# Performance work log

Measured on AMD Instinct MI355X. Metric: run time of the kernel, lower is better.

## Reference

```python
import jax, jax.numpy as jnp
import numpy as np

B, S, D = 4, 2048, 1024
DFF = 4096        # dense FFN hidden
E, DFE = 8, 1024  # n_experts, expert hidden
K = 2             # top-k routing
LAM = 0.5         # coe_lambda


def setup_inputs() -> dict:
    key = jax.random.key(0)
    ks = jax.random.split(key, 10)
    s = 0.02
    return {
        "x":   jax.random.normal(ks[0], (B, S, D), jnp.float32),
        "W1":  jax.random.normal(ks[1], (D, DFF), jnp.float32) * s,
        "b1":  jnp.zeros((DFF,), jnp.float32),
        "W2":  jax.random.normal(ks[2], (DFF, D), jnp.float32) * s,
        "b2":  jnp.zeros((D,), jnp.float32),
        "Wg":  jax.random.normal(ks[3], (D, E), jnp.float32) * s,
        "We1": jax.random.normal(ks[4], (E, D, DFE), jnp.float32) * s,
        "be1": jnp.zeros((E, DFE), jnp.float32),
        "We2": jax.random.normal(ks[5], (E, DFE, D), jnp.float32) * s,
        "be2": jnp.zeros((E, D), jnp.float32),
        "id":  S // 2,  # python int cutoff: tokens < id are FFN-only
    }


def reference(x, W1, b1, W2, b2, Wg, We1, be1, We2, be2, id):
    # Dense FFN applied to every token (both branches compute it).
    ffn_out = jax.nn.gelu(x @ W1 + b1) @ W2 + b2                   # [B,S,D]

    # MoE: softmax router, top-k renormalized gates.
    probs = jax.nn.softmax(x @ Wg, axis=-1)                        # [B,S,E]
    topv, topi = jax.lax.top_k(probs, K)                           # [B,S,K]
    topv = topv / topv.sum(-1, keepdims=True)
    gates = (jax.nn.one_hot(topi, E, dtype=x.dtype) * topv[..., None]).sum(-2)  # [B,S,E]

    # All-expert dense evaluation, then gated combine.
    h = jax.nn.gelu(jnp.einsum('bsd,edf->bsef', x, We1) + be1)     # [B,S,E,DFE]
    eo = jnp.einsum('bsef,efd->bsed', h, We2) + be2                # [B,S,E,D]
    moe_out = jnp.einsum('bse,bsed->bsd', gates, eo)               # [B,S,D]

    # Branch selection: token i < id (and S != 1) -> FFN only; else FFN + lam*MoE.
    seq = x.shape[1]
    mask = ((jnp.arange(seq) >= id) | (seq == 1)).astype(x.dtype)  # [S]
    return ffn_out + LAM * mask[None, :, None] * moe_out
```

## Files before the change

kernel.cpp:

```cpp
#include <hip/hip_runtime.h>
#include <hip/hip_bf16.h>
#include <cstdint>
#include <cstddef>

typedef unsigned short ushort_t;
typedef __bf16 bf16x8v __attribute__((ext_vector_type(8)));
typedef float f32x4 __attribute__((ext_vector_type(4)));

#define Bsz 4
#define Sseq 2048
#define Dd 1024
#define DFFd 4096
#define Ee 8
#define DFEd 1024
#define IDCUT 1024
#define NTOK (Bsz*Sseq)
#define NMOE (Bsz*(Sseq-IDCUT))
#define MAXSLOT 4096

__device__ __forceinline__ ushort_t f2bf(float f) {
  unsigned u = __float_as_uint(f);
  u += 0x7fffu + ((u >> 16) & 1u);
  return (ushort_t)(u >> 16);
}

__device__ __forceinline__ unsigned pk2bf(float a, float b) {
  return (unsigned)f2bf(a) | ((unsigned)f2bf(b) << 16);
}

__device__ __forceinline__ float gelu_f(float x) {
  float u = x * (1.0f + 0.044715f * x * x);
  float s = 1.0f / (1.0f + __expf(-1.5957691216057308f * u));
  return x * s;
}

__device__ __forceinline__ void gload_lds16(const void* g, void* l) {
  __builtin_amdgcn_global_load_lds(
      (const __attribute__((address_space(1))) void*)g,
      (__attribute__((address_space(3))) void*)l,
      16, 0, 0);
}

__device__ __forceinline__ void cast_dev(const float* __restrict__ x,
                                         ushort_t* __restrict__ xb, int wg) {
  const int row  = wg * 4 + (threadIdx.x >> 6);
  const int lane = threadIdx.x & 63;
  const float* xr = x + (size_t)row * Dd;
  ushort_t* xbr = xb + (size_t)row * Dd;
  float4 v[4];
  #pragma unroll
  for (int j = 0; j < 4; ++j) v[j] = ((const float4*)xr)[lane + j * 64];
  #pragma unroll
  for (int j = 0; j < 4; ++j) {
    ushort4 o;
    o.x = f2bf(v[j].x); o.y = f2bf(v[j].y); o.z = f2bf(v[j].z); o.w = f2bf(v[j].w);
    ((ushort4*)xbr)[lane + j * 64] = o;
  }
}

__device__ __forceinline__ void router_dev(
    const float* __restrict__ x, const float* __restrict__ Wg,
    int* __restrict__ cnt, int* __restrict__ slots, float* __restrict__ gsv,
    int blk, int* __restrict__ eTok, int* __restrict__ lbase)
{
  const int wid = threadIdx.x >> 6, lane = threadIdx.x & 63;
  const int tblk = blk * 64;

  #pragma unroll 1
  for (int it = 0; it < 16; ++it) {
    const int ti = it * 4 + wid;
    const int t  = tblk + ti;
    const int b  = t >> 10, s = (t & 1023) + IDCUT;
    const float* xr = x + ((size_t)b * Sseq + s) * Dd;
    float4 accA = {0.f,0.f,0.f,0.f}, accB = {0.f,0.f,0.f,0.f};
    #pragma unroll
    for (int j = 0; j < 4; ++j) {
      const float4 v = ((const float4*)xr)[lane + j * 64];
      const int kbase = (lane + j * 64) * 4;
      #pragma unroll
      for (int r = 0; r < 4; ++r) {
        const float xv = (r == 0) ? v.x : (r == 1) ? v.y : (r == 2) ? v.z : v.w;
        const float4 wa = *(const float4*)(Wg + (size_t)(kbase + r) * 8);
        const float4 wb = *(const float4*)(Wg + (size_t)(kbase + r) * 8 + 4);
        accA.x += xv * wa.x; accA.y += xv * wa.y; accA.z += xv * wa.z; accA.w += xv * wa.w;
        accB.x += xv * wb.x; accB.y += xv * wb.y; accB.z += xv * wb.z; accB.w += xv * wb.w;
      }
    }
    float acc[8] = {accA.x, accA.y, accA.z, accA.w, accB.x, accB.y, accB.z, accB.w};
    #pragma unroll
    for (int off = 32; off > 0; off >>= 1) {
      #pragma unroll
      for (int e8 = 0; e8 < 8; ++e8) acc[e8] += __shfl_xor(acc[e8], off);
    }
    if (lane == 0) {
      int e0 = 0; float v0 = acc[0];
      #pragma unroll
      for (int e8 = 1; e8 < 8; ++e8) if (acc[e8] > v0) { v0 = acc[e8]; e0 = e8; }
      int e1 = -1; float v1 = -3.4e38f;
      #pragma unroll
      for (int e8 = 0; e8 < 8; ++e8) if (e8 != e0 && acc[e8] > v1) { v1 = acc[e8]; e1 = e8; }
      float g0 = 1.0f / (1.0f + expf(v1 - v0));
      eTok[ti * 2] = e0; eTok[ti * 2 + 1] = e1;
      gsv[t * 2] = g0;  gsv[t * 2 + 1] = 1.0f - g0;
    }
  }
  __syncthreads();
  if (wid == 0) {
    int cnts[8] = {0,0,0,0,0,0,0,0};
    int el[2];
    #pragma unroll
    for (int p = 0; p < 2; ++p) {
      el[p] = eTok[p * 64 + lane];
      #pragma unroll
      for (int e = 0; e < 8; ++e)
        cnts[e] += __popcll(__ballot(el[p] == e));
    }
    if (lane < 8) lbase[lane] = atomicAdd(&cnt[lane], cnts[lane]);
    int run[8];
    #pragma unroll
    for (int e = 0; e < 8; ++e) run[e] = lbase[e];
    #pragma unroll
    for (int p = 0; p < 2; ++p) {
      const int ent = p * 64 + lane;
      const int val = (tblk + (ent >> 1)) * 2 + (ent & 1);
      #pragma unroll
      for (int e = 0; e < 8; ++e) {
        unsigned long long m = __ballot(el[p] == e);
        if (el[p] == e)
          slots[e * MAXSLOT + run[e] + __popcll(m & ((1ull << lane) - 1ull))] = val;
        run[e] += __popcll(m);
      }
    }
  }
}

__device__ __forceinline__ void t64x128(const float* __restrict__ in,
                                        ushort_t* __restrict__ out,
                                        int R, int C, int by, int bx,
                                        float* __restrict__ lds) {
  const int t = threadIdx.x;
  const int c4 = t & 31;
  const int r0 = t >> 5;
  const float* src = in + (size_t)(by * 64) * C + bx * 128;
  #pragma unroll
  for (int p = 0; p < 8; ++p) {
    const int r = r0 + p * 8;
    const float4 vv = *(const float4*)(src + (size_t)r * C + c4 * 4);
    *(float4*)(lds + r * 129 + c4 * 4) = vv;
  }
  __syncthreads();
  ushort_t* dst = out + (size_t)(bx * 128) * R + by * 64;
  const int rr0 = (t & 7) * 8;
  #pragma unroll
  for (int p = 0; p < 4; ++p) {
    const int cc = (t >> 3) + p * 32;
    const float* col = lds + (size_t)rr0 * 129 + cc;
    float f0 = col[0*129], f1 = col[1*129], f2 = col[2*129], f3 = col[3*129];
    float f4 = col[4*129], f5 = col[5*129], f6 = col[6*129], f7 = col[7*129];
    uint4 q;
    q.x = pk2bf(f0, f1); q.y = pk2bf(f2, f3);
    q.z = pk2bf(f4, f5); q.w = pk2bf(f6, f7);
    *(uint4*)(dst + (size_t)cc * R + rr0) = q;
  }
}

__global__ __launch_bounds__(256) void prep1_k(
    const float* __restrict__ x, ushort_t* __restrict__ xb,
    const float* __restrict__ Wg,
    int* __restrict__ cnt, int* __restrict__ slots, float* __restrict__ gsv,
    const float* __restrict__ W1, ushort_t* __restrict__ W1t,
    const float* __restrict__ We1, ushort_t* __restrict__ We1t)
{
  __shared__ char smemraw[64 * 129 * 4];
  const int wg = blockIdx.x;
  if (wg < 2048) {
    cast_dev(x, xb, wg);
  } else if (wg < 2112) {
    router_dev(x, Wg, cnt, slots, gsv, wg - 2048,
               (int*)smemraw, (int*)(smemraw + 512));
  } else if (wg < 2624) {
    const int i = wg - 2112;
    t64x128(W1, W1t, Dd, DFFd, i >> 5, i & 31, (float*)smemraw);
  } else {
    const int i = wg - 2624, z = i >> 7, rem = i & 127;
    t64x128(We1 + (size_t)z * Dd * DFEd, We1t + (size_t)z * Dd * DFEd,
            Dd, DFEd, rem >> 3, rem & 7, (float*)smemraw);
  }
}

template<int MODE>
__device__ __forceinline__ void gemm_tile(
    int nt, int mt, int e,
    const ushort_t* __restrict__ A, const ushort_t* __restrict__ Bt,
    const float* __restrict__ biase, void* __restrict__ C,
    int M, int lda, int N, int ldc,
    const int* __restrict__ cnt, const int* __restrict__ slots,
    const float* __restrict__ gates,
    ushort_t* Al, ushort_t* Bl)
{
  int rows = M;
  const int* slist = nullptr;
  if (MODE >= 2) {
    rows = cnt[e];
    if (mt * 128 >= rows) return;
    slist = slots + e * MAXSLOT;
  }
  const ushort_t* Bte = (MODE >= 2) ? (Bt + (size_t)e * (size_t)lda * (size_t)N) : Bt;

  const int tid  = threadIdx.x;
  const int lane = tid & 63;
  const int wid  = tid >> 6;
  const int wr   = wid >> 1, wc = wid & 1;
  const int lr   = lane & 15;
  const int lg   = lane >> 4;
  const int swz7 = lane & 7;

  const ushort_t* gA[4];
  const ushort_t* gB[4];
  #pragma unroll
  for (int j = 0; j < 4; ++j) {
    int tt = j * 256 + tid;
    int rl = tt >> 3, slot = tt & 7;
    int col8 = slot ^ (rl & 7);
    int grow = mt * 128 + rl;
    size_t rowoff;
    if (MODE < 2) {
      rowoff = (size_t)grow;
    } else {
      int idx = grow > rows - 1 ? rows - 1 : grow;
      int sv = slist[idx];
      if (MODE == 2) { int t = sv >> 1; rowoff = (size_t)((t >> 10) * Sseq + IDCUT + (t & 1023)); }
      else           { rowoff = (size_t)sv; }
    }
    gA[j] = A + rowoff * (size_t)lda + col8 * 8;
    gB[j] = Bte + (size_t)(nt * 128 + rl) * (size_t)lda + col8 * 8;
  }

  f32x4 acc[4][4];
  const f32x4 vzero = {0.f, 0.f, 0.f, 0.f};
  #pragma unroll
  for (int m = 0; m < 4; ++m)
    #pragma unroll
    for (int n = 0; n < 4; ++n) acc[m][n] = vzero;

  const unsigned aRow = (unsigned)((wr * 64 + lr) * 128);
  const unsigned bRow = (unsigned)((wc * 64 + lr) * 128);
  const unsigned s0 = (unsigned)((lg ^ swz7) << 4);
  const unsigned s1 = (unsigned)(((4 + lg) ^ swz7) << 4);

  for (int k0 = 0; k0 < lda; k0 += 64) {
    __syncthreads();
    #pragma unroll
    for (int j = 0; j < 4; ++j)
      gload_lds16(gA[j] + k0, (void*)((char*)Al + (j * 256 + wid * 64) * 16));
    #pragma unroll
    for (int j = 0; j < 4; ++j)
      gload_lds16(gB[j] + k0, (void*)((char*)Bl + (j * 256 + wid * 64) * 16));
    __syncthreads();

    {
      bf16x8v af[4], bfr[4];
      #pragma unroll
      for (int mi = 0; mi < 4; ++mi)
        af[mi] = *(const bf16x8v*)((const char*)Al + aRow + mi * 2048 + s0);
      #pragma unroll
      for (int ni = 0; ni < 4; ++ni)
        bfr[ni] = *(const bf16x8v*)((const char*)Bl + bRow + ni * 2048 + s0);
      #pragma unroll
      for (int mi = 0; mi < 4; ++mi)
        #pragma unroll
        for (int ni = 0; ni < 4; ++ni)
          acc[mi][ni] = __builtin_amdgcn_mfma_f32_16x16x32_bf16(
              af[mi], bfr[ni], acc[mi][ni], 0, 0, 0);
    }
    {
      bf16x8v af[4], bfr[4];
      #pragma unroll
      for (int mi = 0; mi < 4; ++mi)
        af[mi] = *(const bf16x8v*)((const char*)Al + aRow + mi * 2048 + s1);
      #pragma unroll
      for (int ni = 0; ni < 4; ++ni)
        bfr[ni] = *(const bf16x8v*)((const char*)Bl + bRow + ni * 2048 + s1);
      #pragma unroll
      for (int mi = 0; mi < 4; ++mi)
        #pragma unroll
        for (int ni = 0; ni < 4; ++ni)
          acc[mi][ni] = __builtin_amdgcn_mfma_f32_16x16x32_bf16(
              af[mi], bfr[ni], acc[mi][ni], 0, 0, 0);
    }
  }

  #pragma unroll
  for (int mf = 0; mf < 4; ++mf) {
    #pragma unroll
    for (int jj = 0; jj < 4; ++jj) {
      const int lrow = wr * 64 + mf * 16 + lg * 4 + jj;
      const int grow = mt * 128 + lrow;
      size_t crow; float gt = 0.f;
      if (MODE >= 2) {
        if (grow >= rows) continue;
        int sv = slist[grow];
        if (MODE == 3) {
          gt = gates[sv];
          int tkn = sv >> 1;
          crow = (size_t)((tkn >> 10) * Sseq + IDCUT + (tkn & 1023));
        } else {
          crow = (size_t)sv;
        }
      } else {
        crow = (size_t)grow;
      }
      #pragma unroll
      for (int nf = 0; nf < 4; ++nf) {
        const int gcol = nt * 128 + wc * 64 + nf * 16 + lr;
        float v = acc[mf][nf][jj] + biase[gcol];
        if (MODE == 0 || MODE == 2) {
          ((ushort_t*)C)[crow * (size_t)ldc + gcol] = f2bf(gelu_f(v));
        } else if (MODE == 1) {
          ((float*)C)[crow * (size_t)ldc + gcol] = v;
        } else {
          atomicAdd(&((float*)C)[crow * (size_t)ldc + gcol], 0.5f * gt * v);
        }
      }
    }
  }
}

__global__ __launch_bounds__(256, 3) void fused1_k(
    const ushort_t* __restrict__ xb,
    const ushort_t* __restrict__ W1t, const float* __restrict__ b1, ushort_t* __restrict__ h1,
    const ushort_t* __restrict__ We1t, const float* __restrict__ be1, ushort_t* __restrict__ hs,
    const int* __restrict__ cnt, const int* __restrict__ slots,
    const float* __restrict__ W2, ushort_t* __restrict__ W2t,
    const float* __restrict__ We2, ushort_t* __restrict__ We2t)
{
  __shared__ char smemraw[64 * 129 * 4];
  ushort_t* Al = (ushort_t*)smemraw;
  ushort_t* Bl = (ushort_t*)(smemraw + 16384);
  int wg = blockIdx.x;
  if (wg < 2048) {
    int xcd = wg & 7, idx = wg >> 3;
    int ntB = idx >> 6, mtL = (idx >> 3) & 7, ntS = idx & 7;
    int mt = xcd * 8 + mtL, nt = ntB * 8 + ntS;
    gemm_tile<0>(nt, mt, 0, xb, W1t, b1, (void*)h1, NTOK, Dd, DFFd, DFFd,
                 nullptr, nullptr, nullptr, Al, Bl);
  } else if (wg < 4096) {
    int i = wg - 2048;
    int e = i & 7, j = i >> 3;
    int mt = j >> 3, nt = j & 7;
    gemm_tile<2>(nt, mt, e, xb, We1t, be1 + e * DFEd, (void*)hs, 0, Dd, DFEd, DFEd,
                 cnt, slots, nullptr, Al, Bl);
  } else if (wg < 4608) {
    const int i = wg - 4096;
    t64x128(W2, W2t, DFFd, Dd, i >> 3, i & 7, (float*)smemraw);
  } else {
    const int i = wg - 4608, z = i >> 7, rem = i & 127;
    t64x128(We2 + (size_t)z * DFEd * Dd, We2t + (size_t)z * DFEd * Dd,
            DFEd, Dd, rem >> 3, rem & 7, (float*)smemraw);
  }
}

__global__ __launch_bounds__(256, 3) void ffn2_k(
    const ushort_t* __restrict__ h1,
    const ushort_t* __restrict__ W2t, const float* __restrict__ b2,
    float* __restrict__ out)
{
  __shared__ ushort_t Al[128 * 64];
  __shared__ ushort_t Bl[128 * 64];
  int wg = blockIdx.x;
  int xcd = wg & 7, idx = wg >> 3;
  int nt = idx >> 3, mtL = idx & 7;
  int mt = xcd * 8 + mtL;
  gemm_tile<1>(nt, mt, 0, h1, W2t, b2, (void*)out, NTOK, DFFd, Dd, Dd,
               nullptr, nullptr, nullptr, Al, Bl);
}

__global__ __launch_bounds__(256, 3) void moe2_k(
    const ushort_t* __restrict__ hs,
    const ushort_t* __restrict__ We2t, const float* __restrict__ be2,
    float* __restrict__ out,
    const int* __restrict__ cnt, const int* __restrict__ slots,
    const float* __restrict__ gsv)
{
  __shared__ ushort_t Al[128 * 64];
  __shared__ ushort_t Bl[128 * 64];
  int wg = blockIdx.x;
  int e = wg & 7, j = wg >> 3;
  int mt = j >> 3, nt = j & 7;
  gemm_tile<3>(nt, mt, e, hs, We2t, be2 + e * Dd, (void*)out, 0, DFEd, Dd, Dd,
               cnt, slots, gsv, Al, Bl);
}

#define WS_XB    ((size_t)0)
#define WS_W1T   ((size_t)16777216)
#define WS_W2T   ((size_t)25165824)
#define WS_WE1T  ((size_t)33554432)
#define WS_WE2T  ((size_t)50331648)
#define WS_H1    ((size_t)67108864)
#define WS_HS    ((size_t)134217728)
#define WS_CNT   ((size_t)184549376)
#define WS_SLOT  ((size_t)184549632)
#define WS_GSV   ((size_t)184680704)

extern "C" void kernel_launch(void* const* d_in, const int* in_sizes, int n_in,
                              void* d_out, int out_size, void* d_ws, size_t ws_size,
                              hipStream_t stream) {
  const float* x   = (const float*)d_in[0];
  const float* W1  = (const float*)d_in[1];
  const float* b1  = (const float*)d_in[2];
  const float* W2  = (const float*)d_in[3];
  const float* b2  = (const float*)d_in[4];
  const float* Wg  = (const float*)d_in[5];
  const float* We1 = (const float*)d_in[6];
  const float* be1 = (const float*)d_in[7];
  const float* We2 = (const float*)d_in[8];
  const float* be2 = (const float*)d_in[9];
  float* out = (float*)d_out;

  char* ws = (char*)d_ws;
  ushort_t* xb   = (ushort_t*)(ws + WS_XB);
  ushort_t* W1t  = (ushort_t*)(ws + WS_W1T);
  ushort_t* W2t  = (ushort_t*)(ws + WS_W2T);
  ushort_t* We1t = (ushort_t*)(ws + WS_WE1T);
  ushort_t* We2t = (ushort_t*)(ws + WS_WE2T);
  ushort_t* h1   = (ushort_t*)(ws + WS_H1);
  ushort_t* hs   = (ushort_t*)(ws + WS_HS);
  int*      cnt  = (int*)(ws + WS_CNT);
  int*      slots= (int*)(ws + WS_SLOT);
  float*    gsv  = (float*)(ws + WS_GSV);

  hipMemsetAsync(cnt, 0, 8 * sizeof(int), stream);

  prep1_k<<<dim3(3648), 256, 0, stream>>>(x, xb, Wg, cnt, slots, gsv,
                                          W1, W1t, We1, We1t);
  fused1_k<<<dim3(5632), 256, 0, stream>>>(xb, W1t, b1, h1, We1t, be1, hs,
                                           cnt, slots, W2, W2t, We2, We2t);
  ffn2_k<<<dim3(512), 256, 0, stream>>>(h1, W2t, b2, out);
  moe2_k<<<dim3(2048), 256, 0, stream>>>(hs, We2t, be2, out, cnt, slots, gsv);
}
```

Before: 292.9 us.

## Merge FFN2 and MoE2 GEMMs into one launch; replace atomics with staged combine

```diff
diff --git a/kernel.cpp b/kernel.cpp
--- a/kernel.cpp
+++ b/kernel.cpp
@@ -300,13 +300,8 @@
       if (MODE >= 2) {
         if (grow >= rows) continue;
         int sv = slist[grow];
-        if (MODE == 3) {
-          gt = gates[sv];
-          int tkn = sv >> 1;
-          crow = (size_t)((tkn >> 10) * Sseq + IDCUT + (tkn & 1023));
-        } else {
-          crow = (size_t)sv;
-        }
+        crow = (size_t)sv;
+        if (MODE == 3) gt = gates[sv];
       } else {
         crow = (size_t)grow;
       }
@@ -319,7 +314,7 @@
         } else if (MODE == 1) {
           ((float*)C)[crow * (size_t)ldc + gcol] = v;
         } else {
-          atomicAdd(&((float*)C)[crow * (size_t)ldc + gcol], 0.5f * gt * v);
+          ((float*)C)[crow * (size_t)ldc + gcol] = gt * v;
         }
       }
     }
@@ -360,35 +355,50 @@
   }
 }
 
-__global__ __launch_bounds__(256, 3) void ffn2_k(
+__global__ __launch_bounds__(256, 3) void fused2_k(
     const ushort_t* __restrict__ h1,
     const ushort_t* __restrict__ W2t, const float* __restrict__ b2,
-    float* __restrict__ out)
+    float* __restrict__ out,
+    const ushort_t* __restrict__ hs,
+    const ushort_t* __restrict__ We2t, const float* __restrict__ be2,
+    float* __restrict__ eo,
+    const int* __restrict__ cnt, const int* __restrict__ slots,
+    const float* __restrict__ gsv)
 {
   __shared__ ushort_t Al[128 * 64];
   __shared__ ushort_t Bl[128 * 64];
   int wg = blockIdx.x;
-  int xcd = wg & 7, idx = wg >> 3;
-  int nt = idx >> 3, mtL = idx & 7;
-  int mt = xcd * 8 + mtL;
-  gemm_tile<1>(nt, mt, 0, h1, W2t, b2, (void*)out, NTOK, DFFd, Dd, Dd,
-               nullptr, nullptr, nullptr, Al, Bl);
-}
-
-__global__ __launch_bounds__(256, 3) void moe2_k(
-    const ushort_t* __restrict__ hs,
-    const ushort_t* __restrict__ We2t, const float* __restrict__ be2,
-    float* __restrict__ out,
-    const int* __restrict__ cnt, const int* __restrict__ slots,
-    const float* __restrict__ gsv)
-{
-  __shared__ ushort_t Al[128 * 64];
-  __shared__ ushort_t Bl[128 * 64];
-  int wg = blockIdx.x;
-  int e = wg & 7, j = wg >> 3;
-  int mt = j >> 3, nt = j & 7;
-  gemm_tile<3>(nt, mt, e, hs, We2t, be2 + e * Dd, (void*)out, 0, DFEd, Dd, Dd,
-               cnt, slots, gsv, Al, Bl);
+  if (wg < 512) {
+    int xcd = wg & 7, idx = wg >> 3;
+    int nt = idx >> 3, mtL = idx & 7;
+    int mt = xcd * 8 + mtL;
+    gemm_tile<1>(nt, mt, 0, h1, W2t, b2, (void*)out, NTOK, DFFd, Dd, Dd,
+                 nullptr, nullptr, nullptr, Al, Bl);
+  } else {
+    int i = wg - 512;
+    int e = i & 7, j = i >> 3;
+    int mt = j >> 3, nt = j & 7;
+    gemm_tile<3>(nt, mt, e, hs, We2t, be2 + e * Dd, (void*)eo, 0, DFEd, Dd, Dd,
+                 cnt, slots, gsv, Al, Bl);
+  }
+}
+
+__global__ __launch_bounds__(256) void combine_k(
+    float* __restrict__ out, const float* __restrict__ eo)
+{
+  int i = blockIdx.x * 256 + threadIdx.x;
+  int t = i >> 8;
+  int c4 = i & 255;
+  size_t r = (size_t)((t >> 10) * Sseq + IDCUT + (t & 1023));
+  const float4 a = ((const float4*)(eo + (size_t)(2 * t) * Dd))[c4];
+  const float4 b = ((const float4*)(eo + (size_t)(2 * t + 1) * Dd))[c4];
+  float4* op = (float4*)(out + r * Dd);
+  float4 o = op[c4];
+  o.x += 0.5f * (a.x + b.x);
+  o.y += 0.5f * (a.y + b.y);
+  o.z += 0.5f * (a.z + b.z);
+  o.w += 0.5f * (a.w + b.w);
+  op[c4] = o;
 }
 
 #define WS_XB    ((size_t)0)
@@ -398,6 +408,7 @@
 #define WS_WE2T  ((size_t)50331648)
 #define WS_H1    ((size_t)67108864)
 #define WS_HS    ((size_t)134217728)
+#define WS_EO    ((size_t)150994944)
 #define WS_CNT   ((size_t)184549376)
 #define WS_SLOT  ((size_t)184549632)
 #define WS_GSV   ((size_t)184680704)
@@ -425,6 +436,7 @@
   ushort_t* We2t = (ushort_t*)(ws + WS_WE2T);
   ushort_t* h1   = (ushort_t*)(ws + WS_H1);
   ushort_t* hs   = (ushort_t*)(ws + WS_HS);
+  float*    eo   = (float*)(ws + WS_EO);
   int*      cnt  = (int*)(ws + WS_CNT);
   int*      slots= (int*)(ws + WS_SLOT);
   float*    gsv  = (float*)(ws + WS_GSV);
@@ -435,6 +447,7 @@
                                           W1, W1t, We1, We1t);
   fused1_k<<<dim3(5632), 256, 0, stream>>>(xb, W1t, b1, h1, We1t, be1, hs,
                                            cnt, slots, W2, W2t, We2, We2t);
-  ffn2_k<<<dim3(512), 256, 0, stream>>>(h1, W2t, b2, out);
-  moe2_k<<<dim3(2048), 256, 0, stream>>>(hs, We2t, be2, out, cnt, slots, gsv);
-}
+  fused2_k<<<dim3(2560), 256, 0, stream>>>(h1, W2t, b2, out,
+                                           hs, We2t, be2, eo, cnt, slots, gsv);
+  combine_k<<<dim3(NMOE * Dd / 4 / 256), 256, 0, stream>>>(out, eo);
+}
```

Result: faster. 279.4 us (-4.6%).
